# Optimization experiments

Measured on AMD Instinct MI355X. Metric: run time of the kernel, lower is better.

Reference implementation:

```python
import jax, jax.numpy as jnp
import numpy as np

N = 100000
E = 1600000
F_IN = 128
HDIM = 64
HEADS = 8
C1 = HDIM // HEADS  # 8 per-head channels in conv1
NUM_CLASSES = 2
NUM_GRAPHS = 64
NEG_SLOPE = 0.2


def setup_inputs() -> dict:
    key = jax.random.key(0)
    ks = jax.random.split(key, 12)
    x = jax.random.normal(ks[0], (N, F_IN), dtype=jnp.float32)
    edge_index = jax.random.randint(ks[1], (2, E), 0, N, dtype=jnp.int64)
    batch = jnp.sort(jax.random.randint(ks[2], (N,), 0, NUM_GRAPHS, dtype=jnp.int64))
    # conv1 params (Glorot-ish scale)
    W1 = jax.random.normal(ks[3], (F_IN, HEADS * C1), dtype=jnp.float32) * (1.0 / np.sqrt(F_IN))
    att_src1 = jax.random.normal(ks[4], (HEADS, C1), dtype=jnp.float32) * 0.1
    att_dst1 = jax.random.normal(ks[5], (HEADS, C1), dtype=jnp.float32) * 0.1
    b1 = jnp.zeros((HEADS * C1,), dtype=jnp.float32)
    # conv2 params (1 head, no concat)
    W2 = jax.random.normal(ks[6], (HDIM, 1 * NUM_CLASSES), dtype=jnp.float32) * (1.0 / np.sqrt(HDIM))
    att_src2 = jax.random.normal(ks[7], (1, NUM_CLASSES), dtype=jnp.float32) * 0.1
    att_dst2 = jax.random.normal(ks[8], (1, NUM_CLASSES), dtype=jnp.float32) * 0.1
    b2 = jnp.zeros((NUM_CLASSES,), dtype=jnp.float32)
    return {"x": x, "edge_index": edge_index, "batch": batch,
            "W1": W1, "att_src1": att_src1, "att_dst1": att_dst1, "b1": b1,
            "W2": W2, "att_src2": att_src2, "att_dst2": att_dst2, "b2": b2}


def gat_conv(x, src, dst, W, a_src, a_dst, b, heads, ch, concat):
    # PyG GATConv: linear proj -> per-edge attention -> segment softmax over dst -> scatter-add
    n = x.shape[0]
    h = (x @ W).reshape(n, heads, ch)                      # [N,H,C]
    alpha_s = jnp.einsum('nhc,hc->nh', h, a_src)           # [N,H]
    alpha_d = jnp.einsum('nhc,hc->nh', h, a_dst)           # [N,H]
    e = jax.nn.leaky_relu(alpha_s[src] + alpha_d[dst], NEG_SLOPE)  # [E,H]
    m = jax.ops.segment_max(e, dst, num_segments=n)        # stable softmax per dst
    e = jnp.exp(e - m[dst])
    denom = jax.ops.segment_sum(e, dst, num_segments=n) + 1e-16
    alpha = e / denom[dst]                                 # [E,H]
    msg = h[src] * alpha[:, :, None]                       # [E,H,C]
    out = jax.ops.segment_sum(msg, dst, num_segments=n)    # [N,H,C]
    if concat:
        out = out.reshape(n, heads * ch)
    else:
        out = out.mean(axis=1)
    return out + b


def reference(x, edge_index, batch, W1, att_src1, att_dst1, b1, W2, att_src2, att_dst2, b2):
    # PyG GATConv default add_self_loops=True
    loops = jnp.arange(N, dtype=edge_index.dtype)
    src = jnp.concatenate([edge_index[0], loops])
    dst = jnp.concatenate([edge_index[1], loops])
    h = gat_conv(x, src, dst, W1, att_src1, att_dst1, b1, HEADS, C1, concat=True)
    h = jax.nn.relu(h)
    # F.dropout with training=False (eval mode) -> identity
    h = gat_conv(h, src, dst, W2, att_src2, att_dst2, b2, 1, NUM_CLASSES, concat=False)
    # global_mean_pool over batch ids
    sums = jax.ops.segment_sum(h, batch, num_segments=NUM_GRAPHS)
    cnts = jax.ops.segment_sum(jnp.ones((N,), h.dtype), batch, num_segments=NUM_GRAPHS)
    pooled = sums / jnp.maximum(cnts, 1.0)[:, None]        # [G, num_classes]
    return jax.nn.log_softmax(pooled, axis=1)
```

## Files before the change

### kernel.cpp

```cpp
#include <hip/hip_runtime.h>
#include <hip/hip_bf16.h>
#include <hip/hip_fp16.h>
#include <math.h>

#define NN 100000
#define EE 1600000
#define ET 1700000
#define NEG_SLOPE 0.2f
#define XS_STRIDE 136
#define L2E 1.44269504088896f

#define BKB 7
#define BKSZ 128
#define NBUCK 782
#define SLAB 4096
#define PAD 32
#define EPT2 16
#define CHUNK2 (256 * EPT2)
#define NCH2 ((ET + CHUNK2 - 1) / CHUNK2)

typedef _Float16 f16;
typedef f16 f16x4 __attribute__((ext_vector_type(4)));
typedef f16 f16x8 __attribute__((ext_vector_type(8)));
typedef float f32x4 __attribute__((ext_vector_type(4)));
typedef float f32x2 __attribute__((ext_vector_type(2)));

__device__ __forceinline__ float leaky(float v) {
    return fmaxf(v, NEG_SLOPE * v);
}
__device__ __forceinline__ unsigned char enc_fp8(float v) {
    int pk = __builtin_amdgcn_cvt_pk_fp8_f32(v, 0.f, 0, false);
    return (unsigned char)(pk & 0xff);
}

__device__ __forceinline__ void fold8(float (&dst)[8], const float (&X)[8],
                                      const float (&Y)[8], int sb, int off) {
#pragma unroll
    for (int i = 0; i < 8; ++i) {
        float m = sb ? Y[i] : X[i];
        float o = sb ? X[i] : Y[i];
        dst[i] = m + __shfl_xor(o, off, 64);
    }
}


__global__ __launch_bounds__(256) void bucket_fill(
        const int* __restrict__ ei, int* __restrict__ bcur,
        unsigned* __restrict__ gpay, const float* __restrict__ W1,
        f16* __restrict__ wt, unsigned char* __restrict__ nrec) {
    const int tid = threadIdx.x;
    if (blockIdx.x < 32) {
        int i = blockIdx.x * 256 + tid;
        int n = i >> 7, k = i & 127;
        wt[n * 128 + k] = (f16)W1[k * 64 + n];
    }
    if (blockIdx.x == 32 && tid < 8) {
        uint4* dr = (uint4*)(nrec + (size_t)NN * 128);
        dr[tid] = make_uint4(0u, 0u, 0xFC00u, 0u);
    }
    __shared__ int lcnt[NBUCK];
    __shared__ int gbase[NBUCK];
    for (int i = tid; i < NBUCK; i += 256) lcnt[i] = 0;
    __syncthreads();
    const int base = blockIdx.x * CHUNK2 + tid;
    unsigned pay[EPT2];
    int bk[EPT2], pos[EPT2];
#pragma unroll
    for (int k = 0; k < EPT2; ++k) {
        int e = base + k * 256;
        if (e < ET) {
            int s, d;
            if (e < EE) {
                s = __builtin_nontemporal_load(ei + e);
                d = __builtin_nontemporal_load(ei + EE + e);
            } else { s = d = e - EE; }
            int b = d >> BKB;
            bk[k] = b;
            pay[k] = ((unsigned)(d & (BKSZ - 1)) << 17) | (unsigned)s;
            pos[k] = atomicAdd(&lcnt[b], 1);
        } else bk[k] = -1;
    }
    __syncthreads();
    for (int i = tid; i < NBUCK; i += 256)
        gbase[i] = lcnt[i] ? (i * SLAB + atomicAdd(&bcur[i * PAD], lcnt[i])) : 0;
    __syncthreads();
#pragma unroll
    for (int k = 0; k < EPT2; ++k)
        if (bk[k] >= 0) gpay[gbase[bk[k]] + pos[k]] = pay[k];
}

__global__ __launch_bounds__(256) void gemm1_mfma(
        const float* __restrict__ x, const f16* __restrict__ wt,
        const float* __restrict__ att_s, const float* __restrict__ att_d,
        unsigned char* __restrict__ nrec) {
    __shared__ f16 xs[64 * XS_STRIDE];
    const int tid = threadIdx.x;
    const int node0 = blockIdx.x * 64;
    for (int i = tid; i < 64 * 32; i += 256) {
        int r = i >> 5, cp = i & 31;
        int n = node0 + r;
        float4 v = (n < NN) ? ((const float4*)x)[(long)n * 32 + cp]
                            : make_float4(0.f, 0.f, 0.f, 0.f);
        f16x4 h = {(f16)v.x, (f16)v.y, (f16)v.z, (f16)v.w};
        *(f16x4*)(xs + r * XS_STRIDE + 4 * cp) = h;
    }
    __syncthreads();
    const int wv = tid >> 6;
    const int lane = tid & 63;
    const int n16 = lane & 15;
    const int quad = lane >> 4;
    f16x8 bf[4][4];
#pragma unroll
    for (int t = 0; t < 4; ++t)
#pragma unroll
        for (int kk = 0; kk < 4; ++kk)
            bf[t][kk] = *(const f16x8*)(wt + ((t * 16 + n16) * 128 + kk * 32 + quad * 8));
    f32x4 acc[4] = {{0,0,0,0},{0,0,0,0},{0,0,0,0},{0,0,0,0}};
#pragma unroll
    for (int kk = 0; kk < 4; ++kk) {
        f16x8 af = *(const f16x8*)(xs + ((wv * 16 + n16) * XS_STRIDE + kk * 32 + quad * 8));
#pragma unroll
        for (int t = 0; t < 4; ++t)
            acc[t] = __builtin_amdgcn_mfma_f32_16x16x32_f16(af, bf[t][kk], acc[t], 0, 0, 0);
    }
    float ats[4], atd[4];
#pragma unroll
    for (int t = 0; t < 4; ++t) {
        ats[t] = att_s[t * 16 + n16];
        atd[t] = att_d[t * 16 + n16];
    }
    const int head = (n16 >> 3);
    const int chpos = n16 & 7;
#pragma unroll
    for (int t = 0; t < 4; ++t)
#pragma unroll
        for (int r = 0; r < 4; ++r) {
            int m = node0 + wv * 16 + quad * 4 + r;
            bool ok = (m < NN);
            if (ok)
                nrec[(size_t)m * 128 + (t * 2 + head) * 16 + chpos] =
                    enc_fp8(acc[t][r]);
            float vs = acc[t][r] * ats[t];
            float vd = acc[t][r] * atd[t];
            vs += __shfl_xor(vs, 1, 64); vd += __shfl_xor(vd, 1, 64);
            vs += __shfl_xor(vs, 2, 64); vd += __shfl_xor(vd, 2, 64);
            vs += __shfl_xor(vs, 4, 64); vd += __shfl_xor(vd, 4, 64);
            if (ok && chpos == 0) {
                unsigned char* nb = nrec + (size_t)m * 128 + (t * 2 + head) * 16;
                *(__half*)(nb + 8)  = __float2half_rn(vs * L2E);
                *(float*)(nb + 12) = vd * L2E;
            }
        }
}

__global__ __launch_bounds__(256) void fine_csr(
        const unsigned* __restrict__ gpay, const int* __restrict__ bcur,
        int* __restrict__ rowptr, int* __restrict__ rowend,
        int* __restrict__ csr_src) {
    __shared__ int cnt[BKSZ];
    __shared__ int ts[256];
    const int b = blockIdx.x;
    const int tid = threadIdx.x;
    const int off = b * SLAB;
    int blen = bcur[b * PAD];
    if (blen > SLAB) blen = SLAB;
    const int d0 = b << BKB;
    if (tid < BKSZ) cnt[tid] = 0;
    __syncthreads();
    for (int i = tid; i < blen; i += 256)
        atomicAdd(&cnt[gpay[off + i] >> 17], 1);
    __syncthreads();
    int v = (tid < BKSZ) ? cnt[tid] : 0;
    int vp = (v + 7) & ~7;
    ts[tid] = vp;
    __syncthreads();
    for (int o = 1; o < 256; o <<= 1) {
        int u = (tid >= o) ? ts[tid - o] : 0;
        __syncthreads();
        ts[tid] += u;
        __syncthreads();
    }
    int excl = ts[tid] - vp;
    if (excl + vp > SLAB) vp = v;
    if (tid < BKSZ) cnt[tid] = excl;
    int d = d0 + tid;
    if (tid < BKSZ && d < NN) {
        rowptr[d] = off + excl;
        rowend[d] = off + excl + v;
    }
    for (int i = v; i < vp; ++i) csr_src[off + excl + i] = NN;
    __syncthreads();
    for (int i = tid; i < blen; i += 256) {
        unsigned pay = gpay[off + i];
        int pos = atomicAdd(&cnt[pay >> 17], 1);
        csr_src[off + pos] = (int)(pay & 0x1FFFFu);
    }
}

__global__ __launch_bounds__(256) void conv1_fused_kernel(
        const int* __restrict__ rowptr, const int* __restrict__ rowend,
        const int* __restrict__ csr_src, const unsigned char* __restrict__ nrec,
        const float* __restrict__ b1, const float* __restrict__ W2,
        const float* __restrict__ as2, const float* __restrict__ ad2,
        float4* __restrict__ rec) {
    const int tid = threadIdx.x;
    const int wv = tid >> 6;
    const int c = tid & 63;
    const int slot = c >> 3;
    const int hd = c & 7;
    const int sb0 = slot & 1, sb1 = (slot >> 1) & 1, sb2 = (slot >> 2) & 1;
    int n0 = __builtin_amdgcn_readfirstlane((blockIdx.x * 4 + wv) * 4);
    const float adA = *(const float*)(nrec + ((size_t)(n0 + 0) << 7) + (hd << 4) + 12);
    const float adB = *(const float*)(nrec + ((size_t)(n0 + 1) << 7) + (hd << 4) + 12);
    const float adC = *(const float*)(nrec + ((size_t)(n0 + 2) << 7) + (hd << 4) + 12);
    const float adD = *(const float*)(nrec + ((size_t)(n0 + 3) << 7) + (hd << 4) + 12);
    int jA = rowptr[n0 + 0], eA = jA + ((rowend[n0 + 0] - jA + 7) & ~7);
    int jB = rowptr[n0 + 1], eB = jB + ((rowend[n0 + 1] - jB + 7) & ~7);
    int jC = rowptr[n0 + 2], eC = jC + ((rowend[n0 + 2] - jC + 7) & ~7);
    int jD = rowptr[n0 + 3], eD = jD + ((rowend[n0 + 3] - jD + 7) & ~7);
    float accA[8] = {0,0,0,0,0,0,0,0}, accB[8] = {0,0,0,0,0,0,0,0};
    float accC[8] = {0,0,0,0,0,0,0,0}, accD[8] = {0,0,0,0,0,0,0,0};
    float lA = 0.f, lB = 0.f, lC = 0.f, lD = 0.f;

#define STEP(j, e, ad, l, acc)                                               \
    {                                                                        \
        int jj = (j) < (e) - 8 ? (j) : (e) - 8;        \
        int src = csr_src[jj + slot];                                        \
        uint4 v = *(const uint4*)(nrec + (((size_t)src << 7) | (hd << 4)));  \
        unsigned short ush = (unsigned short)v.z;                            \
        float as = __half2float(*(const __half*)&ush);                       \
        float p = exp2f(leaky(as + (ad)));                                   \
        p = ((j) < (e)) ? p : 0.f;                                           \
        f32x2 f01 = __builtin_amdgcn_cvt_pk_f32_fp8((int)v.x, 0);            \
        f32x2 f23 = __builtin_amdgcn_cvt_pk_f32_fp8((int)v.x, 1);            \
        f32x2 f45 = __builtin_amdgcn_cvt_pk_f32_fp8((int)v.y, 0);            \
        f32x2 f67 = __builtin_amdgcn_cvt_pk_f32_fp8((int)v.y, 1);            \
        (l) += p;                                                            \
        acc[0] += p * f01.x; acc[1] += p * f01.y;                            \
        acc[2] += p * f23.x; acc[3] += p * f23.y;                            \
        acc[4] += p * f45.x; acc[5] += p * f45.y;                            \
        acc[6] += p * f67.x; acc[7] += p * f67.y;                            \
        (j) += 8;                                                            \
    }

    while (jA < eA || jB < eB || jC < eC || jD < eD) {
        STEP(jA, eA, adA, lA, accA);
        STEP(jB, eB, adB, lB, accB);
        STEP(jC, eC, adC, lC, accC);
        STEP(jD, eD, adD, lD, accD);
    }
#undef STEP

    float P[8], Q[8];
    fold8(P, accA, accB, sb0, 8);
    fold8(Q, accC, accD, sb0, 8);
    float lP, lQ, lm, lo;
    lm = sb0 ? lB : lA; lo = sb0 ? lA : lB;
    lP = lm + __shfl_xor(lo, 8, 64);
    lm = sb0 ? lD : lC; lo = sb0 ? lC : lD;
    lQ = lm + __shfl_xor(lo, 8, 64);
    float R[8];
    fold8(R, P, Q, sb1, 16);
    lm = sb1 ? lQ : lP; lo = sb1 ? lP : lQ;
    float l = lm + __shfl_xor(lo, 16, 64);
    float S[4];
#pragma unroll
    for (int i = 0; i < 4; ++i) {
        float m = sb2 ? R[i + 4] : R[i];
        float o = sb2 ? R[i] : R[i + 4];
        S[i] = m + __shfl_xor(o, 32, 64);
    }
    l += __shfl_xor(l, 32, 64);
    const int cb = (hd << 3) + sb2 * 4;
    float inv = 1.f / (l + 1e-16f);
    float4 bb = *(const float4*)(b1 + cb);
    float4 w01 = *(const float4*)(W2 + cb * 2);
    float4 w23 = *(const float4*)(W2 + cb * 2 + 4);
    float v0 = fmaxf(S[0] * inv + bb.x, 0.f);
    float v1 = fmaxf(S[1] * inv + bb.y, 0.f);
    float v2 = fmaxf(S[2] * inv + bb.z, 0.f);
    float v3 = fmaxf(S[3] * inv + bb.w, 0.f);
    float r0 = v0 * w01.x + v1 * w01.z + v2 * w23.x + v3 * w23.z;
    float r1 = v0 * w01.y + v1 * w01.w + v2 * w23.y + v3 * w23.w;
    r0 += __shfl_xor(r0, 1, 64);  r1 += __shfl_xor(r1, 1, 64);
    r0 += __shfl_xor(r0, 2, 64);  r1 += __shfl_xor(r1, 2, 64);
    r0 += __shfl_xor(r0, 4, 64);  r1 += __shfl_xor(r1, 4, 64);
    r0 += __shfl_xor(r0, 32, 64); r1 += __shfl_xor(r1, 32, 64);
    if (hd == 0 && sb2 == 0) {
        int n = n0 + sb1 * 2 + sb0;
        rec[n] = make_float4((r0 * as2[0] + r1 * as2[1]) * L2E, r0, r1,
                             (r0 * ad2[0] + r1 * ad2[1]) * L2E);
    }
}

__global__ __launch_bounds__(256) void conv2_pool_kernel(
        const int* __restrict__ rowptr, const int* __restrict__ rowend,
        const int* __restrict__ csr_src, const float4* __restrict__ rec,
        const int* __restrict__ batch,
        float* __restrict__ pooled ) {
    __shared__ float ls[192];
    int tid = threadIdx.x;
    if (tid < 192) ls[tid] = 0.f;
    __syncthreads();
    int n = blockIdx.x * 256 + tid;
    if (n < NN) {
        float adn = rec[n].w;
        int jb = rowptr[n], je = rowend[n];
        float l0 = 0.f, l1 = 0.f, l2 = 0.f, l3 = 0.f;
        float x0 = 0.f, x1 = 0.f, x2 = 0.f, x3 = 0.f;
        float y0 = 0.f, y1 = 0.f, y2 = 0.f, y3 = 0.f;
        int j = jb;
        int i0 = csr_src[j], i1 = csr_src[j + 1];
        int i2 = csr_src[j + 2], i3 = csr_src[j + 3];
        for (; j + 3 < je; ) {
            float4 ra = rec[i0];
            float4 rb = rec[i1];
            float4 rc = rec[i2];
            float4 rd = rec[i3];
            j += 4;
            i0 = csr_src[j] & 0x1FFFF;     i1 = csr_src[j + 1] & 0x1FFFF;
            i2 = csr_src[j + 2] & 0x1FFFF; i3 = csr_src[j + 3] & 0x1FFFF;
            float pa = exp2f(leaky(ra.x + adn));
            float pb = exp2f(leaky(rb.x + adn));
            float pc = exp2f(leaky(rc.x + adn));
            float pd = exp2f(leaky(rd.x + adn));
            l0 += pa; x0 += pa * ra.y; y0 += pa * ra.z;
            l1 += pb; x1 += pb * rb.y; y1 += pb * rb.z;
            l2 += pc; x2 += pc * rc.y; y2 += pc * rc.z;
            l3 += pd; x3 += pd * rd.y; y3 += pd * rd.z;
        }
        for (; j < je; ++j) {
            float4 ra = rec[csr_src[j]];
            float pa = exp2f(leaky(ra.x + adn));
            l0 += pa; x0 += pa * ra.y; y0 += pa * ra.z;
        }
        float l = (l0 + l1) + (l2 + l3);
        float xx = (x0 + x1) + (x2 + x3);
        float yy = (y0 + y1) + (y2 + y3);
        float inv = 1.f / (l + 1e-16f);
        int g = batch[n];
        atomicAdd(&ls[g * 2],     xx * inv);
        atomicAdd(&ls[g * 2 + 1], yy * inv);
        atomicAdd(&ls[128 + g],   1.f);
    }
    __syncthreads();
    if (tid < 192) atomicAdd(&pooled[tid], ls[tid]);
}

__global__ __launch_bounds__(64) void final_kernel(
        const float* __restrict__ pooled, const float* __restrict__ b2,
        float* __restrict__ out) {
    int g = threadIdx.x;
    if (g >= 64) return;
    float c = pooled[128 + g];
    float denom = c > 1.f ? c : 1.f;
    float p0 = pooled[g * 2] / denom + b2[0];
    float p1 = pooled[g * 2 + 1] / denom + b2[1];
    float m = fmaxf(p0, p1);
    float lse = m + logf(expf(p0 - m) + expf(p1 - m));
    out[g * 2] = p0 - lse;
    out[g * 2 + 1] = p1 - lse;
}

extern "C" void kernel_launch(void* const* d_in, const int* in_sizes, int n_in,
                              void* d_out, int out_size, void* d_ws, size_t ws_size,
                              hipStream_t stream) {
    const float* x   = (const float*)d_in[0];
    const int*   ei  = (const int*)d_in[1];
    const int*   bat = (const int*)d_in[2];
    const float* W1  = (const float*)d_in[3];
    const float* as1 = (const float*)d_in[4];
    const float* ad1 = (const float*)d_in[5];
    const float* b1  = (const float*)d_in[6];
    const float* W2  = (const float*)d_in[7];
    const float* as2 = (const float*)d_in[8];
    const float* ad2 = (const float*)d_in[9];
    const float* b2  = (const float*)d_in[10];
    float* out = (float*)d_out;

    float* ws = (float*)d_ws;
    const long off_nrec   = 0;
    const long off_wt     = off_nrec + (long)(NN + 1) * 32;
    const long off_rec    = off_wt + 4096;
    const long off_rowptr = off_rec + (long)NN * 4;
    const long off_rowend = off_rowptr + NN;
    const long off_gpay   = off_rowend + NN;
    const long off_csr    = off_gpay + (long)NBUCK * SLAB;
    const long off_zero   = off_csr + (long)NBUCK * SLAB;
    const long off_bcur   = off_zero;
    const long off_pool   = off_bcur + (long)NBUCK * PAD;
    const long zero_elems = off_pool + 192 - off_zero;

    hipMemsetAsync(ws + off_zero, 0, zero_elems * sizeof(float), stream);

    bucket_fill<<<NCH2, 256, 0, stream>>>(
        ei, (int*)(ws + off_bcur), (unsigned*)(ws + off_gpay),
        W1, (f16*)(ws + off_wt), (unsigned char*)(ws + off_nrec));

    gemm1_mfma<<<(NN + 63) / 64, 256, 0, stream>>>(
        x, (const f16*)(ws + off_wt), as1, ad1,
        (unsigned char*)(ws + off_nrec));

    fine_csr<<<NBUCK, 256, 0, stream>>>(
        (const unsigned*)(ws + off_gpay), (const int*)(ws + off_bcur),
        (int*)(ws + off_rowptr), (int*)(ws + off_rowend),
        (int*)(ws + off_csr));

    conv1_fused_kernel<<<NN / 16, 256, 0, stream>>>(
        (const int*)(ws + off_rowptr), (const int*)(ws + off_rowend),
        (const int*)(ws + off_csr), (const unsigned char*)(ws + off_nrec),
        b1, W2, as2, ad2, (float4*)(ws + off_rec));

    conv2_pool_kernel<<<(NN + 255) / 256, 256, 0, stream>>>(
        (const int*)(ws + off_rowptr), (const int*)(ws + off_rowend),
        (const int*)(ws + off_csr), (const float4*)(ws + off_rec),
        bat, ws + off_pool);

    final_kernel<<<1, 64, 0, stream>>>(ws + off_pool, b2, out);
}
```

Measured before the change: 230.5 us.

## Merge fine CSR build into GEMM launch and split conv2 rows across two lanes

The fine_csr bucket sort and the MFMA projection GEMM are independent, so they now run as one launch. The first NBUCK blocks build the CSR and the remaining blocks do the GEMM, which removes a kernel boundary and lets the two workloads overlap. conv2_pool now gives each destination node two threads that take alternating edges and combine their partial sums with a shuffle. This doubles the thread-level parallelism for the irregular gather, but each thread has fewer loads in flight than with the old 4-way prefetch.

Measured after the change: 240.8 us. +4.5%, slower.

```diff
diff --git a/kernel.cpp b/kernel.cpp
--- a/kernel.cpp
+++ b/kernel.cpp
@@ -18,6 +18,7 @@
 #define EPT2 16
 #define CHUNK2 (256 * EPT2)
 #define NCH2 ((ET + CHUNK2 - 1) / CHUNK2)
+#define GEMM_BLOCKS ((NN + 63) / 64)
 
 typedef _Float16 f16;
 typedef f16 f16x4 __attribute__((ext_vector_type(4)));
@@ -89,13 +90,59 @@
         if (bk[k] >= 0) gpay[gbase[bk[k]] + pos[k]] = pay[k];
 }
 
-__global__ __launch_bounds__(256) void gemm1_mfma(
+__global__ __launch_bounds__(256) void gemm_csr_fused(
+        const unsigned* __restrict__ gpay, const int* __restrict__ bcur,
+        int* __restrict__ rowptr, int* __restrict__ rowend,
+        int* __restrict__ csr_src,
         const float* __restrict__ x, const f16* __restrict__ wt,
         const float* __restrict__ att_s, const float* __restrict__ att_d,
         unsigned char* __restrict__ nrec) {
-    __shared__ f16 xs[64 * XS_STRIDE];
+    __shared__ __align__(16) char smem[64 * XS_STRIDE * 2];
     const int tid = threadIdx.x;
-    const int node0 = blockIdx.x * 64;
+
+    if (blockIdx.x < NBUCK) {
+        int* cnt = (int*)smem;
+        int* ts  = cnt + BKSZ;
+        const int b = blockIdx.x;
+        const int off = b * SLAB;
+        int blen = bcur[b * PAD];
+        if (blen > SLAB) blen = SLAB;
+        const int d0 = b << BKB;
+        if (tid < BKSZ) cnt[tid] = 0;
+        __syncthreads();
+        for (int i = tid; i < blen; i += 256)
+            atomicAdd(&cnt[gpay[off + i] >> 17], 1);
+        __syncthreads();
+        int v = (tid < BKSZ) ? cnt[tid] : 0;
+        int vp = (v + 7) & ~7;
+        ts[tid] = vp;
+        __syncthreads();
+        for (int o = 1; o < 256; o <<= 1) {
+            int u = (tid >= o) ? ts[tid - o] : 0;
+            __syncthreads();
+            ts[tid] += u;
+            __syncthreads();
+        }
+        int excl = ts[tid] - vp;
+        if (excl + vp > SLAB) vp = v;
+        if (tid < BKSZ) cnt[tid] = excl;
+        int d = d0 + tid;
+        if (tid < BKSZ && d < NN) {
+            rowptr[d] = off + excl;
+            rowend[d] = off + excl + v;
+        }
+        for (int i = v; i < vp; ++i) csr_src[off + excl + i] = NN;
+        __syncthreads();
+        for (int i = tid; i < blen; i += 256) {
+            unsigned pay = gpay[off + i];
+            int pos = atomicAdd(&cnt[pay >> 17], 1);
+            csr_src[off + pos] = (int)(pay & 0x1FFFFu);
+        }
+        return;
+    }
+
+    f16* xs = (f16*)smem;
+    const int node0 = (blockIdx.x - NBUCK) * 64;
     for (int i = tid; i < 64 * 32; i += 256) {
         int r = i >> 5, cp = i & 31;
         int n = node0 + r;
@@ -151,50 +198,6 @@
                 *(float*)(nb + 12) = vd * L2E;
             }
         }
-}
-
-__global__ __launch_bounds__(256) void fine_csr(
-        const unsigned* __restrict__ gpay, const int* __restrict__ bcur,
-        int* __restrict__ rowptr, int* __restrict__ rowend,
-        int* __restrict__ csr_src) {
-    __shared__ int cnt[BKSZ];
-    __shared__ int ts[256];
-    const int b = blockIdx.x;
-    const int tid = threadIdx.x;
-    const int off = b * SLAB;
-    int blen = bcur[b * PAD];
-    if (blen > SLAB) blen = SLAB;
-    const int d0 = b << BKB;
-    if (tid < BKSZ) cnt[tid] = 0;
-    __syncthreads();
-    for (int i = tid; i < blen; i += 256)
-        atomicAdd(&cnt[gpay[off + i] >> 17], 1);
-    __syncthreads();
-    int v = (tid < BKSZ) ? cnt[tid] : 0;
-    int vp = (v + 7) & ~7;
-    ts[tid] = vp;
-    __syncthreads();
-    for (int o = 1; o < 256; o <<= 1) {
-        int u = (tid >= o) ? ts[tid - o] : 0;
-        __syncthreads();
-        ts[tid] += u;
-        __syncthreads();
-    }
-    int excl = ts[tid] - vp;
-    if (excl + vp > SLAB) vp = v;
-    if (tid < BKSZ) cnt[tid] = excl;
-    int d = d0 + tid;
-    if (tid < BKSZ && d < NN) {
-        rowptr[d] = off + excl;
-        rowend[d] = off + excl + v;
-    }
-    for (int i = v; i < vp; ++i) csr_src[off + excl + i] = NN;
-    __syncthreads();
-    for (int i = tid; i < blen; i += 256) {
-        unsigned pay = gpay[off + i];
-        int pos = atomicAdd(&cnt[pay >> 17], 1);
-        csr_src[off + pos] = (int)(pay & 0x1FFFFu);
-    }
 }
 
 __global__ __launch_bounds__(256) void conv1_fused_kernel(
@@ -302,46 +305,39 @@
     int tid = threadIdx.x;
     if (tid < 192) ls[tid] = 0.f;
     __syncthreads();
-    int n = blockIdx.x * 256 + tid;
+    int q = tid & 1;
+    int n = blockIdx.x * 128 + (tid >> 1);
     if (n < NN) {
         float adn = rec[n].w;
         int jb = rowptr[n], je = rowend[n];
-        float l0 = 0.f, l1 = 0.f, l2 = 0.f, l3 = 0.f;
-        float x0 = 0.f, x1 = 0.f, x2 = 0.f, x3 = 0.f;
-        float y0 = 0.f, y1 = 0.f, y2 = 0.f, y3 = 0.f;
-        int j = jb;
-        int i0 = csr_src[j], i1 = csr_src[j + 1];
-        int i2 = csr_src[j + 2], i3 = csr_src[j + 3];
-        for (; j + 3 < je; ) {
-            float4 ra = rec[i0];
-            float4 rb = rec[i1];
-            float4 rc = rec[i2];
-            float4 rd = rec[i3];
-            j += 4;
-            i0 = csr_src[j] & 0x1FFFF;     i1 = csr_src[j + 1] & 0x1FFFF;
-            i2 = csr_src[j + 2] & 0x1FFFF; i3 = csr_src[j + 3] & 0x1FFFF;
+        float l0 = 0.f, l1 = 0.f;
+        float x0 = 0.f, x1 = 0.f;
+        float y0 = 0.f, y1 = 0.f;
+        int j = jb + q;
+        for (; j + 2 < je; j += 4) {
+            float4 ra = rec[csr_src[j]];
+            float4 rb = rec[csr_src[j + 2]];
             float pa = exp2f(leaky(ra.x + adn));
             float pb = exp2f(leaky(rb.x + adn));
-            float pc = exp2f(leaky(rc.x + adn));
-            float pd = exp2f(leaky(rd.x + adn));
             l0 += pa; x0 += pa * ra.y; y0 += pa * ra.z;
             l1 += pb; x1 += pb * rb.y; y1 += pb * rb.z;
-            l2 += pc; x2 += pc * rc.y; y2 += pc * rc.z;
-            l3 += pd; x3 += pd * rd.y; y3 += pd * rd.z;
-        }
-        for (; j < je; ++j) {
+        }
+        if (j < je) {
             float4 ra = rec[csr_src[j]];
             float pa = exp2f(leaky(ra.x + adn));
             l0 += pa; x0 += pa * ra.y; y0 += pa * ra.z;
         }
-        float l = (l0 + l1) + (l2 + l3);
-        float xx = (x0 + x1) + (x2 + x3);
-        float yy = (y0 + y1) + (y2 + y3);
-        float inv = 1.f / (l + 1e-16f);
-        int g = batch[n];
-        atomicAdd(&ls[g * 2],     xx * inv);
-        atomicAdd(&ls[g * 2 + 1], yy * inv);
-        atomicAdd(&ls[128 + g],   1.f);
+        float l = l0 + l1, xx = x0 + x1, yy = y0 + y1;
+        l += __shfl_xor(l, 1, 64);
+        xx += __shfl_xor(xx, 1, 64);
+        yy += __shfl_xor(yy, 1, 64);
+        if (q == 0) {
+            float inv = 1.f / (l + 1e-16f);
+            int g = batch[n];
+            atomicAdd(&ls[g * 2],     xx * inv);
+            atomicAdd(&ls[g * 2 + 1], yy * inv);
+            atomicAdd(&ls[128 + g],   1.f);
+        }
     }
     __syncthreads();
     if (tid < 192) atomicAdd(&pooled[tid], ls[tid]);
@@ -397,21 +393,19 @@
         ei, (int*)(ws + off_bcur), (unsigned*)(ws + off_gpay),
         W1, (f16*)(ws + off_wt), (unsigned char*)(ws + off_nrec));
 
-    gemm1_mfma<<<(NN + 63) / 64, 256, 0, stream>>>(
+    gemm_csr_fused<<<NBUCK + GEMM_BLOCKS, 256, 0, stream>>>(
+        (const unsigned*)(ws + off_gpay), (const int*)(ws + off_bcur),
+        (int*)(ws + off_rowptr), (int*)(ws + off_rowend),
+        (int*)(ws + off_csr),
         x, (const f16*)(ws + off_wt), as1, ad1,
         (unsigned char*)(ws + off_nrec));
-
-    fine_csr<<<NBUCK, 256, 0, stream>>>(
-        (const unsigned*)(ws + off_gpay), (const int*)(ws + off_bcur),
-        (int*)(ws + off_rowptr), (int*)(ws + off_rowend),
-        (int*)(ws + off_csr));
 
     conv1_fused_kernel<<<NN / 16, 256, 0, stream>>>(
         (const int*)(ws + off_rowptr), (const int*)(ws + off_rowend),
         (const int*)(ws + off_csr), (const unsigned char*)(ws + off_nrec),
         b1, W2, as2, ad2, (float4*)(ws + off_rec));
 
-    conv2_pool_kernel<<<(NN + 255) / 256, 256, 0, stream>>>(
+    conv2_pool_kernel<<<(NN + 127) / 128, 256, 0, stream>>>(
         (const int*)(ws + off_rowptr), (const int*)(ws + off_rowend),
         (const int*)(ws + off_csr), (const float4*)(ws + off_rec),
         bat, ws + off_pool);
```
